# Kernel tuning notes

Measured on AMD Instinct MI355X. Metric: run time of the kernel, lower is better.

Reference implementation:

```python
import jax, jax.numpy as jnp
import numpy as np

NPERSEG = 512
STEP = 256
NSEG = 9            # frames for L=2048 with boundary='zeros', padded=True
NFREQ = 257
NUM_FILTER = 2
PI = 3.1415926      # same constant as source

_win = 0.5 * (1.0 - jnp.cos(2.0 * jnp.pi * jnp.arange(NPERSEG, dtype=jnp.float32) / NPERSEG))  # periodic hann (scipy get_window('hann'))
_win_sum = 256.0    # sum of periodic hann, exact


def _stft(x):
    # x: (B, D, L) real -> scipy.signal.stft(..., nperseg=512, noverlap=256) => (B, D, 257, 9)
    xp = jnp.pad(x, ((0, 0), (0, 0), (STEP, STEP)))  # boundary='zeros'
    idx = jnp.arange(NSEG)[:, None] * STEP + jnp.arange(NPERSEG)[None, :]
    frames = xp[..., idx] * _win                     # (B,D,9,512)
    Z = jnp.fft.rfft(frames, axis=-1) / _win_sum     # scaling='spectrum'
    return jnp.swapaxes(Z, -1, -2)                   # (B,D,257,9)


def _istft(Z):
    # Z: (B,D,257,9) complex -> (B,D,2048) real (scipy.signal.istft inverse)
    xs = jnp.fft.irfft(jnp.swapaxes(Z, -1, -2) * _win_sum, n=NPERSEG, axis=-1) * _win  # (B,D,9,512)
    total = NPERSEG + (NSEG - 1) * STEP  # 2560
    idx = (jnp.arange(NSEG)[:, None] * STEP + jnp.arange(NPERSEG)[None, :]).reshape(-1)
    B, D = Z.shape[0], Z.shape[1]
    x = jnp.zeros((B, D, total), xs.dtype).at[..., idx].add(xs.reshape(B, D, -1))
    norm = jnp.zeros((total,), jnp.float32).at[idx].add(jnp.tile(_win ** 2, NSEG))
    x = x / jnp.where(norm > 1e-10, norm, 1.0)
    return x[..., STEP:total - STEP]  # trim boundary padding -> length 2048


def _cplx(p):
    return p[..., 0] + 1j * p[..., 1]  # torch.view_as_complex


def _filter(x, length, bank):
    # x: (B,S,D) complex; bank: (K,S,D,2). power = x*x/length (complex square, as in source)
    power = x * x / length
    k = jnp.arange(NUM_FILTER, dtype=jnp.float32)
    coef = jnp.cos((2.0 * (k + 1.0) - 1.0) * PI / 2.0 * NUM_FILTER)  # matches source precedence
    return jnp.sum(power[None] * _cplx(bank)[:, None] * coef[:, None, None, None], axis=0)


def _ln(x, g, b):
    m = jnp.mean(x, -1, keepdims=True)
    v = jnp.mean((x - m) ** 2, -1, keepdims=True)
    return (x - m) * jax.lax.rsqrt(v + 1e-5) * g + b


def _addnorm(x, g1, b1, w1, bb1, w2, bb2, g2, b2):
    x = _ln(x, g1, b1)
    h = jax.nn.gelu(x @ w1.T + bb1, approximate=False)  # torch GELU (exact)
    return _ln(h @ w2.T + bb2 + x, g2, b2)


def setup_inputs() -> dict:
    key = jax.random.key(0)
    ks = jax.random.split(key, 12)
    B, D = 8, 768
    d = {}
    d['ecg'] = jax.random.normal(ks[0], (B, 2048, D), jnp.float32)
    d['image'] = jax.random.normal(ks[1], (B, 196, D), jnp.float32)
    d['ecg_filter_bank'] = jax.random.normal(ks[2], (2, 2313, D, 2), jnp.float32)
    d['cxr_filter_bank'] = jax.random.normal(ks[3], (2, 99, D, 2), jnp.float32)
    d['gate_sel'] = jax.random.normal(ks[4], (99, D, 2), jnp.float32)
    d['gate_w'] = jax.random.normal(ks[5], (D, D), jnp.float32) * 0.02
    d['gate_b'] = jnp.zeros((D,), jnp.float32)
    for i, p in enumerate(['e', 'c']):
        d[p + '_ln1_g'] = jnp.ones((D,), jnp.float32)
        d[p + '_ln1_b'] = jnp.zeros((D,), jnp.float32)
        d[p + '_w1'] = jax.random.normal(ks[6 + 2 * i], (D, D), jnp.float32) * 0.02
        d[p + '_b1'] = jnp.zeros((D,), jnp.float32)
        d[p + '_w2'] = jax.random.normal(ks[7 + 2 * i], (D, D), jnp.float32) * 0.02
        d[p + '_b2'] = jnp.zeros((D,), jnp.float32)
        d[p + '_ln2_g'] = jnp.ones((D,), jnp.float32)
        d[p + '_ln2_b'] = jnp.zeros((D,), jnp.float32)
    return d


def reference(ecg, image, ecg_filter_bank, cxr_filter_bank, gate_sel, gate_w, gate_b,
              e_ln1_g, e_ln1_b, e_w1, e_b1, e_w2, e_b2, e_ln2_g, e_ln2_b,
              c_ln1_g, c_ln1_b, c_w1, c_b1, c_w2, c_b2, c_ln2_g, c_ln2_b):
    B, S, D = ecg.shape
    N = image.shape[1]
    # STFT path (source detaches to CPU -> stop_gradient)
    Z = _stft(jnp.swapaxes(jax.lax.stop_gradient(ecg), 1, 2))       # (B,D,257,9)
    _ecg = jnp.transpose(Z, (0, 2, 3, 1)).reshape(B, NFREQ * NSEG, D)
    _img = jnp.fft.rfft(image, axis=1, norm='ortho')                # (B,99,D)
    _ecg = _filter(_ecg, NFREQ * NSEG, ecg_filter_bank)
    _img = _filter(_img, N // 2 + 1, cxr_filter_bank)
    # Cxr2EcgGate: complex selection, avgpool over spatial (real part), 1x1 conv
    gate = jnp.mean((_img * _cplx(gate_sel)).real, axis=1) @ gate_w.T + gate_b  # (B,D)
    ecg_g = _ecg * gate[:, None, :]
    # NOTE: source overwrites gated image with irfft of filtered _image (ecg_gate output unused)
    img_t = jnp.fft.irfft(_img, n=N, axis=1, norm='ortho')          # (B,N,D)
    Zg = jnp.transpose(ecg_g.reshape(B, NFREQ, NSEG, D), (0, 3, 1, 2))
    ecg_t = jnp.swapaxes(_istft(jax.lax.stop_gradient(Zg)), 1, 2)   # (B,2048,D); source detaches before istft
    text = _addnorm(ecg_t + ecg, e_ln1_g, e_ln1_b, e_w1, e_b1, e_w2, e_b2, e_ln2_g, e_ln2_b)
    img = _addnorm(img_t + image, c_ln1_g, c_ln1_b, c_w1, c_b1, c_w2, c_b2, c_ln2_g, c_ln2_b)
    return (text, img)
```

## Files before the change

kernel.cpp:

```cpp
#include <hip/hip_runtime.h>
#include <math.h>

namespace {

constexpr int B_ = 8;
constexpr int S_ = 2048;
constexpr int D_ = 768;
constexpr int N_ = 196;
constexpr int NF_ = 99;
constexpr int NFREQ_ = 257;
constexpr int NSEG_ = 9;
constexpr int NBINS_ = NFREQ_ * NSEG_;
constexpr int NW_ = D_ * D_;
constexpr float TWOPI_ = 6.28318530717958647692f;

using bf16x8 = __attribute__((ext_vector_type(8))) short;
using f32x4  = __attribute__((ext_vector_type(4))) float;

__device__ __forceinline__ int rev9(int x) { return (int)(__brev((unsigned)x) >> 23); }
__device__ __forceinline__ int padz(int i) { return i + (i >> 4); }

__device__ __forceinline__ unsigned short f2bf(float x) {
  unsigned u = __float_as_uint(x);
  u = (u + 0x7FFFu + ((u >> 16) & 1u)) >> 16;
  return (unsigned short)u;
}
__device__ __forceinline__ float bf2f(unsigned short h) {
  return __uint_as_float(((unsigned)h) << 16);
}

__device__ __forceinline__ float gelu_f(float v) {
  const float x = fabsf(v) * 0.70710678118654752440f;
  const float t = 1.0f / fmaf(0.3275911f, x, 1.0f);
  float p = fmaf(fmaf(fmaf(fmaf(1.061405429f, t, -1.453152027f), t, 1.421413741f),
                      t, -0.284496736f), t, 0.254829592f);
  const float e = __expf(-x * x);
  const float er = 1.0f - p * t * e;
  return 0.5f * v * (1.0f + ((v < 0.f) ? -er : er));
}

__device__ __forceinline__ void gload16(const void* g, void* l) {
  __builtin_amdgcn_global_load_lds((const __attribute__((address_space(1))) void*)g,
                                   (__attribute__((address_space(3))) void*)l, 16, 0, 0);
}

__global__ __launch_bounds__(256) void k_transpose_g(const float* __restrict__ src,
                                                     float* __restrict__ dst,
                                                     int R, int C) {
  __shared__ float tile[32][33];
  const int b = blockIdx.z;
  const int c0 = blockIdx.x * 32;
  const int r0 = blockIdx.y * 32;
  const int tx = threadIdx.x & 31, ty = threadIdx.x >> 5;
  for (int i = ty; i < 32; i += 8)
    tile[i][tx] = src[((size_t)b * R + r0 + i) * C + c0 + tx];
  __syncthreads();
  for (int i = ty; i < 32; i += 8)
    dst[((size_t)b * C + c0 + i) * R + r0 + tx] = tile[tx][i];
}

constexpr int PREP_W = (NW_ + 255) / 256;
constexpr int PREP_WALL = 4 * PREP_W;
constexpr int PREP_FC = (NBINS_ * D_ + 255) / 256;
__global__ __launch_bounds__(256) void k_prep(
    const float* __restrict__ w0, const float* __restrict__ w1,
    const float* __restrict__ w2, const float* __restrict__ w3,
    unsigned short* __restrict__ wbf, const float2* __restrict__ e2,
    float2* __restrict__ FcT, float2* __restrict__ twg) {
  const int bid = blockIdx.x;
  if (bid < PREP_WALL) {
    const int m = bid / PREP_W;
    const int i = (bid - m * PREP_W) * 256 + threadIdx.x;
    if (i >= NW_) return;
    const float* src = (m == 0) ? w0 : (m == 1) ? w1 : (m == 2) ? w2 : w3;
    wbf[(size_t)m * NW_ + i] = f2bf(src[i]);
  } else if (bid < PREP_WALL + PREP_FC) {
    const int o = (bid - PREP_WALL) * 256 + threadIdx.x;
    if (o >= NBINS_ * D_) return;
    const int d = o / NBINS_;
    const int r = o - d * NBINS_;
    const int f = r / NFREQ_;
    const int k = r - f * NFREQ_;
    const int s = k * 9 + f;
    const float2 a = e2[(size_t)s * D_ + d];
    const float2 b = e2[(size_t)(NBINS_ + s) * D_ + d];
    FcT[o] = make_float2(-(a.x + b.x), -(a.y + b.y));
  } else {
    const int i = (bid - PREP_WALL - PREP_FC) * 256 + threadIdx.x;
    if (i >= 511) return;
    const int v = i + 1;
    const int h = 1 << (31 - __clz(v));
    const int j = v - h;
    float sn, cs;
    sincosf((float)j * ((TWOPI_ * 0.5f) / (float)h), &sn, &cs);
    twg[i] = make_float2(cs, sn);
  }
}

__global__ __launch_bounds__(256) void k_img_dft_f(
    const float* __restrict__ image, const float2* __restrict__ bank2,
    const float2* __restrict__ gsel2, float2* __restrict__ imgF,
    float* __restrict__ part) {
  const int fg = blockIdx.x;
  const int f0 = fg * 9;
  const int d = blockIdx.y * 256 + threadIdx.x;
  const int b = blockIdx.z;
  __shared__ float2 tws[9 * N_];
  for (int idx = threadIdx.x; idx < 9 * N_; idx += 256) {
    const int fi = idx / N_;
    const int t = idx - fi * N_;
    const int r = ((f0 + fi) * t) % N_;
    float sn, cs;
    sincosf(TWOPI_ * (float)r / (float)N_, &sn, &cs);
    tws[idx] = make_float2(cs, sn);
  }
  __syncthreads();
  float re[9] = {}, im[9] = {};
  const float* ip = image + (size_t)b * N_ * D_ + d;
  for (int t = 0; t < N_; ++t) {
    const float v = ip[(size_t)t * D_];
#pragma unroll
    for (int fi = 0; fi < 9; ++fi) {
      const float2 w = tws[fi * N_ + t];
      re[fi] = fmaf(v, w.x, re[fi]);
      im[fi] = fmaf(-v, w.y, im[fi]);
    }
  }
  const float sc = 1.0f / (196.0f * 99.0f);
  float gp = 0.f;
#pragma unroll
  for (int fi = 0; fi < 9; ++fi) {
    const int f = f0 + fi;
    const float pr = (re[fi] * re[fi] - im[fi] * im[fi]) * sc;
    const float pi2 = (2.f * re[fi] * im[fi]) * sc;
    const size_t fd = (size_t)f * D_ + d;
    const float2 c0 = bank2[fd];
    const float2 c1 = bank2[(size_t)NF_ * D_ + fd];
    const float fcr = -(c0.x + c1.x), fci = -(c0.y + c1.y);
    const float zr = pr * fcr - pi2 * fci;
    const float zi = pr * fci + pi2 * fcr;
    imgF[(size_t)(b * NF_ + f) * D_ + d] = make_float2(zr, zi);
    const float2 gw = gsel2[fd];
    gp += zr * gw.x - zi * gw.y;
  }
  part[((size_t)b * 11 + fg) * D_ + d] = gp;
}

__global__ __launch_bounds__(256) void k_gate_mm2(const float* __restrict__ part,
                                                  const float* __restrict__ W,
                                                  const float* __restrict__ bias,
                                                  float* __restrict__ gate) {
  __shared__ float row[8][D_];
  __shared__ float red[16][16][8];
  const int tid = threadIdx.x;
  const int d0 = blockIdx.x * 16;
  for (int i = tid; i < 8 * D_; i += 256) {
    const int b = i / D_, e = i - b * D_;
    float s = 0.f;
    for (int p = 0; p < 11; ++p) s += part[((size_t)b * 11 + p) * D_ + e];
    row[b][e] = s * (1.0f / 99.0f);
  }
  __syncthreads();
  const int dl = tid >> 4;
  const int ec = tid & 15;
  const float* w = W + (size_t)(d0 + dl) * D_ + ec * 48;
  float acc[8] = {};
  for (int e = 0; e < 48; e += 4) {
    const float4 wv = *reinterpret_cast<const float4*>(w + e);
    const int eg = ec * 48 + e;
#pragma unroll
    for (int b = 0; b < 8; ++b) {
      acc[b] = fmaf(row[b][eg], wv.x, acc[b]);
      acc[b] = fmaf(row[b][eg + 1], wv.y, acc[b]);
      acc[b] = fmaf(row[b][eg + 2], wv.z, acc[b]);
      acc[b] = fmaf(row[b][eg + 3], wv.w, acc[b]);
    }
  }
#pragma unroll
  for (int b = 0; b < 8; ++b) red[dl][ec][b] = acc[b];
  __syncthreads();
  if (tid < 128) {
    const int dl2 = tid >> 3, b = tid & 7;
    float s = bias[d0 + dl2];
    for (int c = 0; c < 16; ++c) s += red[dl2][c][b];
    gate[b * D_ + d0 + dl2] = s;
  }
}

__global__ __launch_bounds__(256) void k_img_idft(
    const float2* __restrict__ imgF, const float* __restrict__ image,
    float* __restrict__ xi) {
  const int t0 = blockIdx.x * 14;
  const int d = blockIdx.y * 256 + threadIdx.x;
  const int b = blockIdx.z;
  __shared__ float2 tws[14 * NF_];
  for (int idx = threadIdx.x; idx < 14 * NF_; idx += 256) {
    const int ti = idx / NF_;
    const int f = idx - ti * NF_;
    const int r = ((t0 + ti) * f) % N_;
    float sn, cs;
    sincosf(TWOPI_ * (float)r / (float)N_, &sn, &cs);
    tws[idx] = make_float2(cs, sn);
  }
  __syncthreads();
  const float2* zp = imgF + (size_t)b * NF_ * D_ + d;
  const float2 z0 = zp[0];
  const float2 zny = zp[(size_t)(NF_ - 1) * D_];
  float acc[14];
#pragma unroll
  for (int ti = 0; ti < 14; ++ti)
    acc[ti] = z0.x + (((t0 + ti) & 1) ? -zny.x : zny.x);
  for (int f = 1; f < NF_ - 1; ++f) {
    const float2 z = zp[(size_t)f * D_];
#pragma unroll
    for (int ti = 0; ti < 14; ++ti) {
      const float2 w = tws[ti * NF_ + f];
      acc[ti] += 2.f * (z.x * w.x - z.y * w.y);
    }
  }
#pragma unroll
  for (int ti = 0; ti < 14; ++ti) {
    const size_t idx = (size_t)(b * N_ + t0 + ti) * D_ + d;
    xi[idx] = acc[ti] * (1.0f / 14.0f) + image[idx];
  }
}

__global__ __launch_bounds__(256) void k_layernorm_f2b(const float* __restrict__ x,
                                                       const float* __restrict__ g,
                                                       const float* __restrict__ b,
                                                       unsigned short* __restrict__ out) {
  const int row = blockIdx.x;
  const int tid = threadIdx.x;
  const float* xr = x + (size_t)row * D_;
  const float v0 = xr[tid], v1 = xr[tid + 256], v2 = xr[tid + 512];
  float s = v0 + v1 + v2;
  float q = v0 * v0 + v1 * v1 + v2 * v2;
  __shared__ float red[8];
  for (int off = 32; off > 0; off >>= 1) {
    s += __shfl_down(s, off);
    q += __shfl_down(q, off);
  }
  if ((tid & 63) == 0) { red[tid >> 6] = s; red[4 + (tid >> 6)] = q; }
  __syncthreads();
  s = red[0] + red[1] + red[2] + red[3];
  q = red[4] + red[5] + red[6] + red[7];
  const float mean = s * (1.0f / 768.0f);
  const float var = q * (1.0f / 768.0f) - mean * mean;
  const float inv = rsqrtf(var + 1e-5f);
  unsigned short* orow = out + (size_t)row * D_;
  orow[tid]       = f2bf((v0 - mean) * inv * g[tid]       + b[tid]);
  orow[tid + 256] = f2bf((v1 - mean) * inv * g[tid + 256] + b[tid + 256]);
  orow[tid + 512] = f2bf((v2 - mean) * inv * g[tid + 512] + b[tid + 512]);
}

template <int SS, int DIR>
__device__ __forceinline__ void dblpass(float2* z, int q, float2 tw1, float2 tw2) {
  asm volatile("s_waitcnt lgkmcnt(0)" ::: "memory");
  const int h = 1 << SS;
  const int j = q & (h - 1);
  const int base = ((q >> SS) << (SS + 2)) | j;
  const int e0 = padz(base), e1 = padz(base + h);
  const int e2 = padz(base + 2 * h), e3 = padz(base + 3 * h);
  const float2 x0 = z[e0], x1 = z[e1], x2 = z[e2], x3 = z[e3];
  const float sg = (DIR < 0) ? -1.f : 1.f;
  const float w1c = tw1.x, w1s = sg * tw1.y;
  const float w2c = tw2.x, w2s = sg * tw2.y;
  const float t1r = x1.x * w1c - x1.y * w1s, t1i = x1.x * w1s + x1.y * w1c;
  const float t3r = x3.x * w1c - x3.y * w1s, t3i = x3.x * w1s + x3.y * w1c;
  const float a0r = x0.x + t1r, a0i = x0.y + t1i;
  const float a1r = x0.x - t1r, a1i = x0.y - t1i;
  const float a2r = x2.x + t3r, a2i = x2.y + t3i;
  const float a3r = x2.x - t3r, a3i = x2.y - t3i;
  const float u2r = a2r * w2c - a2i * w2s, u2i = a2r * w2s + a2i * w2c;
  const float v3r = a3r * w2c - a3i * w2s, v3i = a3r * w2s + a3i * w2c;
  const float u3r = -sg * v3i, u3i = sg * v3r;
  z[e0] = make_float2(a0r + u2r, a0i + u2i);
  z[e2] = make_float2(a0r - u2r, a0i - u2i);
  z[e1] = make_float2(a1r + u3r, a1i + u3i);
  z[e3] = make_float2(a1r - u3r, a1i - u3i);
}

template <int DIR>
__device__ __forceinline__ void stage8(float2* z, float2 t8, int t) {
  const float wc = t8.x, ws = (DIR < 0) ? -t8.y : t8.y;
  const int a0 = padz(t), a1 = padz(t + 256);
  const float2 x = z[a0], y = z[a1];
  const float tr = y.x * wc - y.y * ws, ti = y.x * ws + y.y * wc;
  z[a0] = make_float2(x.x + tr, x.y + ti);
  z[a1] = make_float2(x.x - tr, x.y - ti);
}

template <int FA, int FB>
__device__ __forceinline__ void filt_pack(const float2* z, int k, float g,
                                          float2 cA, float2 cB,
                                          float2& Ck, float2& Cm) {
  const int q = (512 - k) & 511;
  const float2 Zk = z[padz(k)], Zq = z[padz(q)];
  const float sc = 0.5f / 256.f;
  const float ar = (Zk.x + Zq.x) * sc, ai = (Zk.y - Zq.y) * sc;
  float yar, yai, ybr = 0.f, ybi = 0.f;
  {
    const float pr = (ar * ar - ai * ai) * (1.f / 2313.f);
    const float pi = (2.f * ar * ai) * (1.f / 2313.f);
    yar = (pr * cA.x - pi * cA.y) * g;
    yai = (pr * cA.y + pi * cA.x) * g;
  }
  if (FB >= 0) {
    const float br = (Zk.y + Zq.y) * sc, bi = (Zq.x - Zk.x) * sc;
    const float pr = (br * br - bi * bi) * (1.f / 2313.f);
    const float pi = (2.f * br * bi) * (1.f / 2313.f);
    ybr = (pr * cB.x - pi * cB.y) * g;
    ybi = (pr * cB.y + pi * cB.x) * g;
  }
  if (k == 0 || k == 256) {
    Ck = make_float2(yar, ybr);
    Cm = Ck;
  } else {
    Ck = make_float2(yar - ybi, yai + ybr);
    Cm = make_float2(yar + ybi, ybr - yai);
  }
}

template <int FA0, int FB0, int FA1, int FB1, bool DUAL>
__device__ __forceinline__ void ecg_super(int tid, float g, const float2* __restrict__ fc,
                                          const float (&s)[8], const float2 (&rt)[4][2],
                                          float2 t8, float2* zA, float2* zB, float* accr) {
  const float c0 = t8.x;
  const float wlo = 0.5f - 0.5f * c0;
  const float whi = 0.5f + 0.5f * c0;
  const float2 cA0 = fc[FA0 * 257 + tid];
  float2 cB0 = make_float2(0.f, 0.f), cA1 = cB0, cB1 = cB0;
  if (FB0 >= 0) cB0 = fc[FB0 * 257 + tid];
  if (DUAL) { cA1 = fc[FA1 * 257 + tid]; cB1 = fc[FB1 * 257 + tid]; }
  float2 nA0 = make_float2(0.f, 0.f), nB0 = nA0, nA1 = nA0, nB1 = nA0;
  if (tid == 0) {
    nA0 = fc[FA0 * 257 + 256];
    if (FB0 >= 0) nB0 = fc[FB0 * 257 + 256];
    if (DUAL) { nA1 = fc[FA1 * 257 + 256]; nB1 = fc[FB1 * 257 + 256]; }
  }
  __syncthreads();
  {
    constexpr int iAlo = (FA0 > 0) ? FA0 - 1 : 0;
    constexpr int iAhi = (FA0 < 8) ? FA0 : 0;
    constexpr int iBlo = (FB0 > 0) ? FB0 - 1 : 0;
    constexpr int iBhi = (FB0 >= 0 && FB0 < 8) ? FB0 : 0;
    const int rlo = padz(rev9(tid)), rhi = padz(rev9(tid + 256));
    const float aLo = (FA0 == 0) ? 0.f : s[iAlo] * wlo;
    const float aHi = (FA0 == 8) ? 0.f : s[iAhi] * whi;
    const float bLo = (FB0 <= 0) ? 0.f : s[iBlo] * wlo;
    const float bHi = (FB0 < 0 || FB0 == 8) ? 0.f : s[iBhi] * whi;
    zA[rlo] = make_float2(aLo, bLo);
    zA[rhi] = make_float2(aHi, bHi);
    if (DUAL) {
      constexpr int jAlo = (FA1 > 0) ? FA1 - 1 : 0;
      constexpr int jAhi = (FA1 < 8) ? FA1 : 0;
      constexpr int jBlo = (FB1 > 0) ? FB1 - 1 : 0;
      constexpr int jBhi = (FB1 < 8) ? FB1 : 0;
      const float eLo = (FA1 == 0) ? 0.f : s[jAlo] * wlo;
      const float eHi = (FA1 == 8) ? 0.f : s[jAhi] * whi;
      const float fLo = (FB1 == 0) ? 0.f : s[jBlo] * wlo;
      const float fHi = (FB1 == 8) ? 0.f : s[jBhi] * whi;
      zB[rlo] = make_float2(eLo, fLo);
      zB[rhi] = make_float2(eHi, fHi);
    }
  }
  __syncthreads();
  if (DUAL || tid < 128) {
    float2* zz = (tid < 128) ? zA : zB;
    const int q = tid & 127;
    dblpass<0, -1>(zz, q, rt[0][0], rt[0][1]);
    dblpass<2, -1>(zz, q, rt[1][0], rt[1][1]);
    dblpass<4, -1>(zz, q, rt[2][0], rt[2][1]);
    dblpass<6, -1>(zz, q, rt[3][0], rt[3][1]);
  }
  __syncthreads();
  stage8<-1>(zA, t8, tid);
  if (DUAL) stage8<-1>(zB, t8, tid);
  __syncthreads();
  float2 CAk, CAm, CBk, CBm;
  filt_pack<FA0, FB0>(zA, tid, g, cA0, cB0, CAk, CAm);
  float2 CAn, CBn, dum;
  if (tid == 0) filt_pack<FA0, FB0>(zA, 256, g, nA0, nB0, CAn, dum);
  if (DUAL) {
    filt_pack<FA1, FB1>(zB, tid, g, cA1, cB1, CBk, CBm);
    if (tid == 0) filt_pack<FA1, FB1>(zB, 256, g, nA1, nB1, CBn, dum);
  }
  __syncthreads();
  {
    const int rk = padz(rev9(tid));
    zA[rk] = CAk;
    if (DUAL) zB[rk] = CBk;
    if (tid == 0) {
      zA[padz(1)] = CAn;
      if (DUAL) zB[padz(1)] = CBn;
    } else {
      const int rm = padz(rev9(512 - tid));
      zA[rm] = CAm;
      if (DUAL) zB[rm] = CBm;
    }
  }
  __syncthreads();
  if (DUAL || tid < 128) {
    float2* zz = (tid < 128) ? zA : zB;
    const int q = tid & 127;
    dblpass<0, 1>(zz, q, rt[0][0], rt[0][1]);
    dblpass<2, 1>(zz, q, rt[1][0], rt[1][1]);
    dblpass<4, 1>(zz, q, rt[2][0], rt[2][1]);
    dblpass<6, 1>(zz, q, rt[3][0], rt[3][1]);
  }
  __syncthreads();
  stage8<1>(zA, t8, tid);
  if (DUAL) stage8<1>(zB, t8, tid);
  {
    const float2 vLo = zA[padz(tid)], vHi = zA[padz(tid + 256)];
    accr[FA0] += 0.5f * wlo * vLo.x;
    accr[FA0 + 1] += 0.5f * whi * vHi.x;
    if (FB0 >= 0) {
      accr[FB0] += 0.5f * wlo * vLo.y;
      accr[FB0 + 1] += 0.5f * whi * vHi.y;
    }
    if (DUAL) {
      const float2 uLo = zB[padz(tid)], uHi = zB[padz(tid + 256)];
      accr[FA1] += 0.5f * wlo * uLo.x;
      accr[FA1 + 1] += 0.5f * whi * uHi.x;
      accr[FB1] += 0.5f * wlo * uLo.y;
      accr[FB1 + 1] += 0.5f * whi * uHi.y;
    }
  }
}

__global__ __launch_bounds__(256) void k_ecg_fft(
    const float* __restrict__ ecgT, const float2* __restrict__ FcT,
    const float* __restrict__ gate, const float2* __restrict__ twg,
    unsigned short* __restrict__ xtT) {
  const int bd = blockIdx.x;
  const int d = bd % D_;
  const int tid = threadIdx.x;

  __shared__ float2 zA[544], zB[544];

  float s[8];
  const float* src = ecgT + (size_t)bd * S_;
#pragma unroll
  for (int k = 0; k < 8; ++k) s[k] = src[k * 256 + tid];

  float2 rt[4][2];
  const int q = tid & 127;
  rt[0][0] = make_float2(1.f, 0.f);
  rt[0][1] = make_float2(0.f, 1.f);
  rt[1][0] = twg[3 + (q & 3)];
  rt[1][1] = twg[7 + (q & 3)];
  rt[2][0] = twg[15 + (q & 15)];
  rt[2][1] = twg[31 + (q & 15)];
  rt[3][0] = twg[63 + (q & 63)];
  rt[3][1] = twg[127 + (q & 63)];
  const float2 t8 = twg[255 + tid];

  const float g = gate[bd];
  const float2* fc = FcT + (size_t)d * NBINS_;
  float accr[10];
#pragma unroll
  for (int i = 0; i < 10; ++i) accr[i] = 0.f;

  ecg_super<0, 8, 1, 2, true>(tid, g, fc, s, rt, t8, zA, zB, accr);
  ecg_super<3, 4, 5, 6, true>(tid, g, fc, s, rt, t8, zA, zB, accr);
  ecg_super<7, -1, 0, 0, false>(tid, g, fc, s, rt, t8, zA, zB, accr);

  const float c0 = t8.x;
  const float rinv = 1.0f / (0.5f + 0.5f * c0 * c0);
  unsigned short* dst = xtT + (size_t)bd * S_;
#pragma unroll
  for (int i2 = 0; i2 < 8; ++i2)
    dst[i2 * 256 + tid] = f2bf(accr[i2 + 1] * rinv + s[i2]);
}

__global__ __launch_bounds__(256) void k_colstats_bf(const unsigned short* __restrict__ xtT,
                                                     float2* __restrict__ stats) {
  const int b = blockIdx.y;
  const int t0 = blockIdx.x * 128;
  const int tx = threadIdx.x & 63;
  const int ty = threadIdx.x >> 6;
  float s0 = 0.f, q0 = 0.f, s1 = 0.f, q1 = 0.f;
  const unsigned int* base = (const unsigned int*)(xtT + (size_t)b * D_ * S_);
  for (int dd = ty; dd < D_; dd += 4) {
    const unsigned int u = base[(size_t)dd * (S_ / 2) + (t0 >> 1) + tx];
    const float v0 = bf2f((unsigned short)(u & 0xffffu));
    const float v1 = bf2f((unsigned short)(u >> 16));
    s0 += v0; q0 = fmaf(v0, v0, q0);
    s1 += v1; q1 = fmaf(v1, v1, q1);
  }
  __shared__ float sh[4][64][4];
  sh[ty][tx][0] = s0; sh[ty][tx][1] = q0; sh[ty][tx][2] = s1; sh[ty][tx][3] = q1;
  __syncthreads();
  if (ty == 0) {
    s0 = sh[0][tx][0] + sh[1][tx][0] + sh[2][tx][0] + sh[3][tx][0];
    q0 = sh[0][tx][1] + sh[1][tx][1] + sh[2][tx][1] + sh[3][tx][1];
    s1 = sh[0][tx][2] + sh[1][tx][2] + sh[2][tx][2] + sh[3][tx][2];
    q1 = sh[0][tx][3] + sh[1][tx][3] + sh[2][tx][3] + sh[3][tx][3];
    stats[(size_t)b * S_ + t0 + 2 * tx]     = make_float2(s0, q0);
    stats[(size_t)b * S_ + t0 + 2 * tx + 1] = make_float2(s1, q1);
  }
}

__global__ __launch_bounds__(256) void k_transpose_ln(
    const unsigned short* __restrict__ xtT, const float2* __restrict__ stats,
    const float* __restrict__ g, const float* __restrict__ bia,
    unsigned short* __restrict__ xhat) {
  __shared__ float tile[32][33];
  const int b = blockIdx.z;
  const int t0 = blockIdx.x * 32;
  const int d0 = blockIdx.y * 32;
  const int tx = threadIdx.x & 31, ty = threadIdx.x >> 5;
  for (int i = ty; i < 32; i += 8)
    tile[i][tx] = bf2f(xtT[((size_t)b * D_ + d0 + i) * S_ + t0 + tx]);
  __syncthreads();
  const float gv = g[d0 + tx], bv = bia[d0 + tx];
  for (int i = ty; i < 32; i += 8) {
    const float2 st = stats[(size_t)b * S_ + t0 + i];
    const float mean = st.x * (1.0f / 768.0f);
    const float var = st.y * (1.0f / 768.0f) - mean * mean;
    const float inv = rsqrtf(var + 1e-5f);
    xhat[((size_t)b * S_ + t0 + i) * D_ + d0 + tx] =
        f2bf((tile[tx][i] - mean) * inv * gv + bv);
  }
}

__global__ __launch_bounds__(256) void k_layernorm_bf(const unsigned short* __restrict__ x,
                                                      const float* __restrict__ g,
                                                      const float* __restrict__ b,
                                                      float* __restrict__ out) {
  const int row = blockIdx.x;
  const int tid = threadIdx.x;
  const unsigned short* xr = x + (size_t)row * D_;
  const float v0 = bf2f(xr[tid]), v1 = bf2f(xr[tid + 256]), v2 = bf2f(xr[tid + 512]);
  float s = v0 + v1 + v2;
  float q = v0 * v0 + v1 * v1 + v2 * v2;
  __shared__ float red[8];
  for (int off = 32; off > 0; off >>= 1) {
    s += __shfl_down(s, off);
    q += __shfl_down(q, off);
  }
  if ((tid & 63) == 0) { red[tid >> 6] = s; red[4 + (tid >> 6)] = q; }
  __syncthreads();
  s = red[0] + red[1] + red[2] + red[3];
  q = red[4] + red[5] + red[6] + red[7];
  const float mean = s * (1.0f / 768.0f);
  const float var = q * (1.0f / 768.0f) - mean * mean;
  const float inv = rsqrtf(var + 1e-5f);
  float* orow = out + (size_t)row * D_;
  orow[tid]       = (v0 - mean) * inv * g[tid]       + b[tid];
  orow[tid + 256] = (v1 - mean) * inv * g[tid + 256] + b[tid + 256];
  orow[tid + 512] = (v2 - mean) * inv * g[tid + 512] + b[tid + 512];
}

template <int MODE, bool SWZ>
__global__ __launch_bounds__(256) void k_gemm_mfma(
    const unsigned short* __restrict__ Abf, const unsigned short* __restrict__ Wbf,
    const float* __restrict__ bias, const unsigned short* __restrict__ resid,
    unsigned short* __restrict__ outb, int M) {
  __shared__ unsigned short Asm[2][128 * 64];
  __shared__ unsigned short Bsm[2][128 * 64];
  const int tid = threadIdx.x;
  const int lane = tid & 63, wid = tid >> 6;
  const int wr = wid >> 1, wc = wid & 1;
  int bx = blockIdx.x, by = blockIdx.y;
  if (SWZ) {
    const int nwg = gridDim.x * gridDim.y;
    const int bid = by * gridDim.x + bx;
    const int nbid = (bid % 8) * (nwg >> 3) + (bid >> 3);
    bx = nbid % gridDim.x;
    by = nbid / gridDim.x;
  }
  const int n0 = bx * 128, m0 = by * 128;

  auto STAGE = [&](int buf, int kt) {
    const int k0 = kt * 64;
#pragma unroll
    for (int i = 0; i < 4; ++i) {
      const int c = tid + 256 * i;
      const int row = c >> 3, sl = c & 7;
      const int gsl = sl ^ (row & 7);
      gload16(Abf + (size_t)(m0 + row) * 768 + k0 + gsl * 8, &Asm[buf][c * 8]);
      gload16(Wbf + (size_t)(n0 + row) * 768 + k0 + gsl * 8, &Bsm[buf][c * 8]);
    }
  };

  f32x4 acc[4][4] = {};
  STAGE(0, 0);
  for (int kt = 0; kt < 12; ++kt) {
    const int cur = kt & 1;
    if (kt < 11) {
      STAGE(cur ^ 1, kt + 1);
      asm volatile("s_waitcnt vmcnt(8)" ::: "memory");
    } else {
      asm volatile("s_waitcnt vmcnt(0)" ::: "memory");
    }
    __builtin_amdgcn_sched_barrier(0);
    __builtin_amdgcn_s_barrier();
#pragma unroll
    for (int ks = 0; ks < 2; ++ks) {
      bf16x8 af[4], bfv[4];
#pragma unroll
      for (int mi = 0; mi < 4; ++mi) {
        const int row = wr * 64 + mi * 16 + (lane & 15);
        const int sl = (ks * 4 + (lane >> 4)) ^ (row & 7);
        af[mi] = *(const bf16x8*)((const char*)Asm[cur] + row * 128 + sl * 16);
      }
#pragma unroll
      for (int ni = 0; ni < 4; ++ni) {
        const int row = wc * 64 + ni * 16 + (lane & 15);
        const int sl = (ks * 4 + (lane >> 4)) ^ (row & 7);
        bfv[ni] = *(const bf16x8*)((const char*)Bsm[cur] + row * 128 + sl * 16);
      }
#pragma unroll
      for (int mi = 0; mi < 4; ++mi)
#pragma unroll
        for (int ni = 0; ni < 4; ++ni)
          acc[mi][ni] = __builtin_amdgcn_mfma_f32_16x16x32_bf16(af[mi], bfv[ni],
                                                                acc[mi][ni], 0, 0, 0);
    }
    __builtin_amdgcn_sched_barrier(0);
    __builtin_amdgcn_s_barrier();
  }
#pragma unroll
  for (int mi = 0; mi < 4; ++mi) {
#pragma unroll
    for (int ni = 0; ni < 4; ++ni) {
      const int col = n0 + wc * 64 + ni * 16 + (lane & 15);
#pragma unroll
      for (int e = 0; e < 4; ++e) {
        const int row = m0 + wr * 64 + mi * 16 + (lane >> 4) * 4 + e;
        if (row >= M) continue;
        float v = acc[mi][ni][e] + bias[col];
        if (MODE == 0) {
          v = gelu_f(v);
        } else {
          v += bf2f(resid[(size_t)row * 768 + col]);
        }
        outb[(size_t)row * 768 + col] = f2bf(v);
      }
    }
  }
}

}

extern "C" void kernel_launch(void* const* d_in, const int* in_sizes, int n_in,
                              void* d_out, int out_size, void* d_ws, size_t ws_size,
                              hipStream_t stream) {
  (void)in_sizes; (void)n_in; (void)out_size; (void)ws_size;
  const float* ecg     = (const float*)d_in[0];
  const float* image   = (const float*)d_in[1];
  const float* ebank   = (const float*)d_in[2];
  const float* cbank   = (const float*)d_in[3];
  const float* gsel    = (const float*)d_in[4];
  const float* gw      = (const float*)d_in[5];
  const float* gb      = (const float*)d_in[6];
  const float* e_ln1_g = (const float*)d_in[7];
  const float* e_ln1_b = (const float*)d_in[8];
  const float* e_w1    = (const float*)d_in[9];
  const float* e_b1    = (const float*)d_in[10];
  const float* e_w2    = (const float*)d_in[11];
  const float* e_b2    = (const float*)d_in[12];
  const float* e_ln2_g = (const float*)d_in[13];
  const float* e_ln2_b = (const float*)d_in[14];
  const float* c_ln1_g = (const float*)d_in[15];
  const float* c_ln1_b = (const float*)d_in[16];
  const float* c_w1    = (const float*)d_in[17];
  const float* c_b1    = (const float*)d_in[18];
  const float* c_w2    = (const float*)d_in[19];
  const float* c_b2    = (const float*)d_in[20];
  const float* c_ln2_g = (const float*)d_in[21];
  const float* c_ln2_b = (const float*)d_in[22];

  float* out = (float*)d_out;
  float* ws = (float*)d_ws;

  constexpr size_t TXT = (size_t)8 * 2048 * 768;
  constexpr size_t IMG = (size_t)8 * 196 * 768;

  float* A  = ws;
  float* Bb = A + TXT;
  unsigned short* wbf = (unsigned short*)(Bb + TXT);
  unsigned short* ew1b = wbf;
  unsigned short* ew2b = wbf + NW_;
  unsigned short* cw1b = wbf + 2 * NW_;
  unsigned short* cw2b = wbf + 3 * NW_;
  float* gatev = (float*)(wbf + 4 * (size_t)NW_);
  float2* stats = (float2*)(gatev + 8 * 768);
  float* gpart = (float*)(stats + 8 * 2048);
  float2* twg = (float2*)(gpart + 8 * 11 * 768);

  float2* FcT = (float2*)out;

  float* xi = A;
  unsigned short* xh_i = (unsigned short*)(A + IMG);
  unsigned short* h_i  = xh_i + IMG;
  unsigned short* y_ib = h_i + IMG;

  unsigned short* xhat = (unsigned short*)A;
  unsigned short* y_tb = (unsigned short*)A + TXT;
  unsigned short* xtT  = (unsigned short*)Bb;
  unsigned short* h_t  = (unsigned short*)Bb;

  k_prep<<<PREP_WALL + PREP_FC + 2, 256, 0, stream>>>(
      e_w1, e_w2, c_w1, c_w2, wbf, (const float2*)ebank, FcT, twg);

  k_img_dft_f<<<dim3(11, 3, 8), 256, 0, stream>>>(image, (const float2*)cbank,
                                                  (const float2*)gsel,
                                                  (float2*)(A + 2 * IMG), gpart);
  k_gate_mm2<<<48, 256, 0, stream>>>(gpart, gw, gb, gatev);
  k_img_idft<<<dim3(14, 3, 8), 256, 0, stream>>>((const float2*)(A + 2 * IMG), image, xi);
  k_layernorm_f2b<<<1568, 256, 0, stream>>>(xi, c_ln1_g, c_ln1_b, xh_i);
  k_gemm_mfma<0, false><<<dim3(6, 13), 256, 0, stream>>>(xh_i, cw1b, c_b1, nullptr, h_i, 1568);
  k_gemm_mfma<1, false><<<dim3(6, 13), 256, 0, stream>>>(h_i, cw2b, c_b2, xh_i, y_ib, 1568);
  k_layernorm_bf<<<1568, 256, 0, stream>>>(y_ib, c_ln2_g, c_ln2_b, out + TXT);

  k_transpose_g<<<dim3(24, 64, 8), 256, 0, stream>>>(ecg, A, 2048, 768);
  k_ecg_fft<<<8 * 768, 256, 0, stream>>>(A, FcT, gatev, twg, xtT);
  k_colstats_bf<<<dim3(16, 8), 256, 0, stream>>>(xtT, stats);
  k_transpose_ln<<<dim3(64, 24, 8), 256, 0, stream>>>(xtT, stats, e_ln1_g, e_ln1_b, xhat);

  k_gemm_mfma<0, true><<<dim3(6, 128), 256, 0, stream>>>(xhat, ew1b, e_b1, nullptr, h_t, 16384);
  k_gemm_mfma<1, true><<<dim3(6, 128), 256, 0, stream>>>(h_t, ew2b, e_b2, xhat, y_tb, 16384);
  k_layernorm_bf<<<16384, 256, 0, stream>>>(y_tb, e_ln2_g, e_ln2_b, out);
}
```

Before: 483.6 us.

## Replace radix-4 plus radix-2 FFT passes with three radix-8 passes

The 512-point shared-memory FFT in the ECG kernel used four radix-4 double passes plus a final radix-2 stage, each with LDS round trips and barriers. It is replaced by three radix-8 passes done by 64 threads per transform, with precomputed per-lane twiddles. This cuts LDS traffic, the number of synchronisation points and the twiddle multiplies. In exchange only 64 or 128 of the 256 threads do FFT work, which lowers parallelism, and each thread holds more registers.

```diff
diff --git a/kernel.cpp b/kernel.cpp
--- a/kernel.cpp
+++ b/kernel.cpp
@@ -42,6 +42,16 @@
 __device__ __forceinline__ void gload16(const void* g, void* l) {
   __builtin_amdgcn_global_load_lds((const __attribute__((address_space(1))) void*)g,
                                    (__attribute__((address_space(3))) void*)l, 16, 0, 0);
+}
+
+__device__ __forceinline__ float2 cmulf(float2 a, float2 b) {
+  return make_float2(a.x * b.x - a.y * b.y, a.x * b.y + a.y * b.x);
+}
+__device__ __forceinline__ float2 cadd(float2 a, float2 b) {
+  return make_float2(a.x + b.x, a.y + b.y);
+}
+__device__ __forceinline__ float2 csub(float2 a, float2 b) {
+  return make_float2(a.x - b.x, a.y - b.y);
 }
 
 __global__ __launch_bounds__(256) void k_transpose_g(const float* __restrict__ src,
@@ -253,41 +263,54 @@
   orow[tid + 512] = f2bf((v2 - mean) * inv * g[tid + 512] + b[tid + 512]);
 }
 
-template <int SS, int DIR>
-__device__ __forceinline__ void dblpass(float2* z, int q, float2 tw1, float2 tw2) {
+template <int H, int DIR, bool TRIV>
+__device__ __forceinline__ void pass8(float2* z, int l,
+                                      float2 wa, float2 wb, float2 wc) {
   asm volatile("s_waitcnt lgkmcnt(0)" ::: "memory");
-  const int h = 1 << SS;
-  const int j = q & (h - 1);
-  const int base = ((q >> SS) << (SS + 2)) | j;
-  const int e0 = padz(base), e1 = padz(base + h);
-  const int e2 = padz(base + 2 * h), e3 = padz(base + 3 * h);
-  const float2 x0 = z[e0], x1 = z[e1], x2 = z[e2], x3 = z[e3];
   const float sg = (DIR < 0) ? -1.f : 1.f;
-  const float w1c = tw1.x, w1s = sg * tw1.y;
-  const float w2c = tw2.x, w2s = sg * tw2.y;
-  const float t1r = x1.x * w1c - x1.y * w1s, t1i = x1.x * w1s + x1.y * w1c;
-  const float t3r = x3.x * w1c - x3.y * w1s, t3i = x3.x * w1s + x3.y * w1c;
-  const float a0r = x0.x + t1r, a0i = x0.y + t1i;
-  const float a1r = x0.x - t1r, a1i = x0.y - t1i;
-  const float a2r = x2.x + t3r, a2i = x2.y + t3i;
-  const float a3r = x2.x - t3r, a3i = x2.y - t3i;
-  const float u2r = a2r * w2c - a2i * w2s, u2i = a2r * w2s + a2i * w2c;
-  const float v3r = a3r * w2c - a3i * w2s, v3i = a3r * w2s + a3i * w2c;
-  const float u3r = -sg * v3i, u3i = sg * v3r;
-  z[e0] = make_float2(a0r + u2r, a0i + u2i);
-  z[e2] = make_float2(a0r - u2r, a0i - u2i);
-  z[e1] = make_float2(a1r + u3r, a1i + u3i);
-  z[e3] = make_float2(a1r - u3r, a1i - u3i);
-}
-
-template <int DIR>
-__device__ __forceinline__ void stage8(float2* z, float2 t8, int t) {
-  const float wc = t8.x, ws = (DIR < 0) ? -t8.y : t8.y;
-  const int a0 = padz(t), a1 = padz(t + 256);
-  const float2 x = z[a0], y = z[a1];
-  const float tr = y.x * wc - y.y * ws, ti = y.x * ws + y.y * wc;
-  z[a0] = make_float2(x.x + tr, x.y + ti);
-  z[a1] = make_float2(x.x - tr, x.y - ti);
+  const int base = (H == 1) ? (l << 3)
+                 : (H == 8) ? (((l >> 3) << 6) | (l & 7))
+                            : l;
+  const float2 x0 = z[padz(base)],         x1 = z[padz(base + H)];
+  const float2 x2 = z[padz(base + 2 * H)], x3 = z[padz(base + 3 * H)];
+  const float2 x4 = z[padz(base + 4 * H)], x5 = z[padz(base + 5 * H)];
+  const float2 x6 = z[padz(base + 6 * H)], x7 = z[padz(base + 7 * H)];
+  const float2 WA = make_float2(wa.x, sg * wa.y);
+  const float2 WB = make_float2(wb.x, sg * wb.y);
+  const float2 WC = make_float2(wc.x, sg * wc.y);
+  const float2 WBp = make_float2(-sg * WB.y, sg * WB.x);
+  float2 t, u;
+  t = TRIV ? x1 : cmulf(x1, WA); const float2 A0 = cadd(x0, t), A1 = csub(x0, t);
+  t = TRIV ? x3 : cmulf(x3, WA); const float2 A2 = cadd(x2, t), A3 = csub(x2, t);
+  t = TRIV ? x5 : cmulf(x5, WA); const float2 A4 = cadd(x4, t), A5 = csub(x4, t);
+  t = TRIV ? x7 : cmulf(x7, WA); const float2 A6 = cadd(x6, t), A7 = csub(x6, t);
+  t = TRIV ? A2 : cmulf(A2, WB);
+  u = TRIV ? make_float2(-sg * A3.y, sg * A3.x) : cmulf(A3, WBp);
+  const float2 B0 = cadd(A0, t), B2 = csub(A0, t);
+  const float2 B1 = cadd(A1, u), B3 = csub(A1, u);
+  t = TRIV ? A6 : cmulf(A6, WB);
+  u = TRIV ? make_float2(-sg * A7.y, sg * A7.x) : cmulf(A7, WBp);
+  const float2 B4 = cadd(A4, t), B6 = csub(A4, t);
+  const float2 B5 = cadd(A5, u), B7 = csub(A5, u);
+  const float r_ = 0.70710678118654752440f;
+  const float2 F1 = TRIV ? make_float2(r_, sg * r_)
+                         : cmulf(WC, make_float2(r_, sg * r_));
+  const float2 F2 = TRIV ? make_float2(0.f, sg)
+                         : make_float2(-sg * WC.y, sg * WC.x);
+  const float2 F3 = TRIV ? make_float2(-r_, sg * r_)
+                         : cmulf(WC, make_float2(-r_, sg * r_));
+  t = TRIV ? B4 : cmulf(B4, WC);
+  z[padz(base)]         = cadd(B0, t);
+  z[padz(base + 4 * H)] = csub(B0, t);
+  t = cmulf(B5, F1);
+  z[padz(base + H)]     = cadd(B1, t);
+  z[padz(base + 5 * H)] = csub(B1, t);
+  t = cmulf(B6, F2);
+  z[padz(base + 2 * H)] = cadd(B2, t);
+  z[padz(base + 6 * H)] = csub(B2, t);
+  t = cmulf(B7, F3);
+  z[padz(base + 3 * H)] = cadd(B3, t);
+  z[padz(base + 7 * H)] = csub(B3, t);
 }
 
 template <int FA, int FB>
@@ -323,7 +346,7 @@
 
 template <int FA0, int FB0, int FA1, int FB1, bool DUAL>
 __device__ __forceinline__ void ecg_super(int tid, float g, const float2* __restrict__ fc,
-                                          const float (&s)[8], const float2 (&rt)[4][2],
+                                          const float (&s)[8], const float2 (&ptw)[6],
                                           float2 t8, float2* zA, float2* zB, float* accr) {
   const float c0 = t8.x;
   const float wlo = 0.5f - 0.5f * c0;
@@ -365,17 +388,13 @@
     }
   }
   __syncthreads();
-  if (DUAL || tid < 128) {
-    float2* zz = (tid < 128) ? zA : zB;
-    const int q = tid & 127;
-    dblpass<0, -1>(zz, q, rt[0][0], rt[0][1]);
-    dblpass<2, -1>(zz, q, rt[1][0], rt[1][1]);
-    dblpass<4, -1>(zz, q, rt[2][0], rt[2][1]);
-    dblpass<6, -1>(zz, q, rt[3][0], rt[3][1]);
-  }
-  __syncthreads();
-  stage8<-1>(zA, t8, tid);
-  if (DUAL) stage8<-1>(zB, t8, tid);
+  if (tid < 64 || (DUAL && tid >= 128 && tid < 192)) {
+    float2* zz = (tid < 64) ? zA : zB;
+    const int l = tid & 63;
+    pass8<1, -1, true>(zz, l, ptw[0], ptw[1], ptw[2]);
+    pass8<8, -1, false>(zz, l, ptw[0], ptw[1], ptw[2]);
+    pass8<64, -1, false>(zz, l, ptw[3], ptw[4], ptw[5]);
+  }
   __syncthreads();
   float2 CAk, CAm, CBk, CBm;
   filt_pack<FA0, FB0>(zA, tid, g, cA0, cB0, CAk, CAm);
@@ -400,17 +419,14 @@
     }
   }
   __syncthreads();
-  if (DUAL || tid < 128) {
-    float2* zz = (tid < 128) ? zA : zB;
-    const int q = tid & 127;
-    dblpass<0, 1>(zz, q, rt[0][0], rt[0][1]);
-    dblpass<2, 1>(zz, q, rt[1][0], rt[1][1]);
-    dblpass<4, 1>(zz, q, rt[2][0], rt[2][1]);
-    dblpass<6, 1>(zz, q, rt[3][0], rt[3][1]);
-  }
-  __syncthreads();
-  stage8<1>(zA, t8, tid);
-  if (DUAL) stage8<1>(zB, t8, tid);
+  if (tid < 64 || (DUAL && tid >= 128 && tid < 192)) {
+    float2* zz = (tid < 64) ? zA : zB;
+    const int l = tid & 63;
+    pass8<1, 1, true>(zz, l, ptw[0], ptw[1], ptw[2]);
+    pass8<8, 1, false>(zz, l, ptw[0], ptw[1], ptw[2]);
+    pass8<64, 1, false>(zz, l, ptw[3], ptw[4], ptw[5]);
+  }
+  __syncthreads();
   {
     const float2 vLo = zA[padz(tid)], vHi = zA[padz(tid + 256)];
     accr[FA0] += 0.5f * wlo * vLo.x;
@@ -444,16 +460,14 @@
 #pragma unroll
   for (int k = 0; k < 8; ++k) s[k] = src[k * 256 + tid];
 
-  float2 rt[4][2];
-  const int q = tid & 127;
-  rt[0][0] = make_float2(1.f, 0.f);
-  rt[0][1] = make_float2(0.f, 1.f);
-  rt[1][0] = twg[3 + (q & 3)];
-  rt[1][1] = twg[7 + (q & 3)];
-  rt[2][0] = twg[15 + (q & 15)];
-  rt[2][1] = twg[31 + (q & 15)];
-  rt[3][0] = twg[63 + (q & 63)];
-  rt[3][1] = twg[127 + (q & 63)];
+  const int l6 = tid & 63;
+  float2 ptw[6];
+  ptw[0] = twg[7 + (l6 & 7)];
+  ptw[1] = twg[15 + (l6 & 7)];
+  ptw[2] = twg[31 + (l6 & 7)];
+  ptw[3] = twg[63 + l6];
+  ptw[4] = twg[127 + l6];
+  ptw[5] = twg[255 + l6];
   const float2 t8 = twg[255 + tid];
 
   const float g = gate[bd];
@@ -462,9 +476,9 @@
 #pragma unroll
   for (int i = 0; i < 10; ++i) accr[i] = 0.f;
 
-  ecg_super<0, 8, 1, 2, true>(tid, g, fc, s, rt, t8, zA, zB, accr);
-  ecg_super<3, 4, 5, 6, true>(tid, g, fc, s, rt, t8, zA, zB, accr);
-  ecg_super<7, -1, 0, 0, false>(tid, g, fc, s, rt, t8, zA, zB, accr);
+  ecg_super<0, 8, 1, 2, true>(tid, g, fc, s, ptw, t8, zA, zB, accr);
+  ecg_super<3, 4, 5, 6, true>(tid, g, fc, s, ptw, t8, zA, zB, accr);
+  ecg_super<7, -1, 0, 0, false>(tid, g, fc, s, ptw, t8, zA, zB, accr);
 
   const float c0 = t8.x;
   const float rinv = 1.0f / (0.5f + 0.5f * c0 * c0);
```

After: 474.6 us. No clear change (-1.9%).
